# Kernel tuning notes

Hardware: AMD Instinct MI355X
Metric: run time of the kernel (lower is better)

Reference implementation:

```python
import jax, jax.numpy as jnp
import numpy as np

N = 16384
IN_FEATS = 256
OUT_FEATS = 256


def setup_inputs() -> dict:
    key = jax.random.key(0)
    k1, k2, k3, k4 = jax.random.split(key, 4)
    # dense (row-normalized-ish) adjacency; scaled so aggregated values stay O(1)
    graph = jax.random.uniform(k1, (N, N), dtype=jnp.float32) / N
    features = jax.random.normal(k2, (N, IN_FEATS), dtype=jnp.float32)
    # nn.Linear params: W [out, in], b [out]
    W = jax.random.normal(k3, (OUT_FEATS, IN_FEATS), dtype=jnp.float32) / np.sqrt(IN_FEATS)
    b = jax.random.normal(k4, (OUT_FEATS,), dtype=jnp.float32) * 0.01
    return {"graph": graph, "features": features, "W": W, "b": b}


def reference(graph, features, W, b):
    # h = graph @ features  (GCN-style dense neighbor aggregation)
    h = jnp.matmul(graph, features)            # [N, in_feats]
    # linear: h @ W.T + b
    h = jnp.einsum('ni,oi->no', h, W) + b      # [N, out_feats]
    # activation = relu (norm = None)
    return jax.nn.relu(h)
```

## Files before the change

### kernel.cpp

```cpp
#include <hip/hip_runtime.h>
#include <hip/hip_bf16.h>

typedef float f32x4 __attribute__((ext_vector_type(4)));
typedef short short8 __attribute__((ext_vector_type(8)));
typedef __bf16 bf16x8 __attribute__((ext_vector_type(8)));

#define N_TOT 16384
#define FEATS 256
#define BM 256
#define BK 32
#define KSPLIT 4
#define LDA (BK + 8)

static __device__ __forceinline__ ushort f2bf(float f) {
  union { __hip_bfloat16 b; ushort u; } cv;
  cv.b = __float2bfloat16(f);
  return cv.u;
}
static __device__ __forceinline__ float bf2f(ushort u) {
  union { unsigned int i; float f; } c;
  c.i = ((unsigned int)u) << 16;
  return c.f;
}

__global__ __launch_bounds__(256) void k_transpose(const float* __restrict__ feat,
                                                   ushort* __restrict__ fT) {
  __shared__ float tile[64][65];
  const int tx = threadIdx.x & 63, ty = threadIdx.x >> 6;
  const int k0 = blockIdx.x * 64, n0 = blockIdx.y * 64;
#pragma unroll
  for (int j = 0; j < 64; j += 4)
    tile[ty + j][tx] = feat[(size_t)(k0 + ty + j) * FEATS + n0 + tx];
  __syncthreads();
#pragma unroll
  for (int j = 0; j < 64; j += 4)
    fT[(size_t)(n0 + ty + j) * N_TOT + k0 + tx] = f2bf(tile[tx][ty + j]);
}

__global__ __launch_bounds__(256) void k_convw(const float* __restrict__ W,
                                               ushort* __restrict__ Wb) {
  int i = (blockIdx.x * 256 + threadIdx.x) * 4;
  float4 v = *(const float4*)(W + i);
  ushort4 h = { f2bf(v.x), f2bf(v.y), f2bf(v.z), f2bf(v.w) };
  *(ushort4*)(Wb + i) = h;
}

__global__ __launch_bounds__(512) void k_gemm1(const float* __restrict__ graph,
                                               const ushort* __restrict__ fT,
                                               ushort* __restrict__ parts) {
  __shared__ ushort Alds[2][BM][LDA];
  __shared__ ushort Blds[2][FEATS][LDA];
  const int tid = threadIdx.x;
  const int lane = tid & 63, w = tid >> 6;
  const int wm = w >> 2, wn = w & 3;
  const size_t m0 = (size_t)blockIdx.x * BM;
  const int kbase = blockIdx.y * (N_TOT / KSPLIT);
  const int nsteps = (N_TOT / KSPLIT) / BK;

  f32x4 acc[8][4] = {};

  auto stage = [&](int bf, int kk) {
#pragma unroll
    for (int i = 0; i < 4; ++i) {
      const int row = i * 64 + (tid >> 3);
      const int kq = (tid & 7) << 2;
      const float4 v = *(const float4*)(graph + (size_t)(m0 + row) * N_TOT + kk + kq);
      ushort4 h = { f2bf(v.x), f2bf(v.y), f2bf(v.z), f2bf(v.w) };
      *(ushort4*)&Alds[bf][row][kq] = h;
    }
    {
      const int n = tid >> 1;
      const int kq = (tid & 1) << 4;
      const short8 v0 = *(const short8*)(fT + (size_t)n * N_TOT + kk + kq);
      const short8 v1 = *(const short8*)(fT + (size_t)n * N_TOT + kk + kq + 8);
      *(short8*)&Blds[bf][n][kq] = v0;
      *(short8*)&Blds[bf][n][kq + 8] = v1;
    }
  };

  stage(0, kbase);
  __syncthreads();

  for (int step = 0; step < nsteps; ++step) {
    const int cur = step & 1;
    if (step + 1 < nsteps) stage(cur ^ 1, kbase + (step + 1) * BK);

    const int koff = (lane >> 4) << 3;
    const int rsel = lane & 15;
    short8 afr[8];
#pragma unroll
    for (int mf = 0; mf < 8; ++mf)
      afr[mf] = *(const short8*)&Alds[cur][wm * 128 + mf * 16 + rsel][koff];
    short8 bfr[4];
#pragma unroll
    for (int nf = 0; nf < 4; ++nf)
      bfr[nf] = *(const short8*)&Blds[cur][wn * 64 + nf * 16 + rsel][koff];
#pragma unroll
    for (int mf = 0; mf < 8; ++mf)
#pragma unroll
      for (int nf = 0; nf < 4; ++nf)
        acc[mf][nf] = __builtin_amdgcn_mfma_f32_16x16x32_bf16(
            __builtin_bit_cast(bf16x8, afr[mf]), __builtin_bit_cast(bf16x8, bfr[nf]),
            acc[mf][nf], 0, 0, 0);
    __syncthreads();
  }

  ushort* p = parts + (size_t)blockIdx.y * N_TOT * FEATS;
#pragma unroll
  for (int mf = 0; mf < 8; ++mf)
#pragma unroll
    for (int nf = 0; nf < 4; ++nf)
#pragma unroll
      for (int j = 0; j < 4; ++j) {
        const int row = wm * 128 + mf * 16 + ((lane >> 4) << 2) + j;
        const int col = wn * 64 + nf * 16 + (lane & 15);
        p[(m0 + row) * FEATS + col] = f2bf(acc[mf][nf][j]);
      }
}

__global__ __launch_bounds__(256) void k_gemm2(const ushort* __restrict__ parts,
                                               const ushort* __restrict__ Wb,
                                               const float* __restrict__ bias,
                                               float* __restrict__ out) {
  __shared__ ushort Al[64][264];
  __shared__ ushort Bl[FEATS][40];
  const int tid = threadIdx.x;
  const int lane = tid & 63, w = tid >> 6;
  const size_t m0 = (size_t)blockIdx.x * 64;

  for (int c = tid; c < 2048; c += 256) {
    const int row = c >> 5;
    const int k8 = (c & 31) << 3;
    const size_t off = (m0 + row) * FEATS + k8;
    float s[8] = {0, 0, 0, 0, 0, 0, 0, 0};
#pragma unroll
    for (int p = 0; p < KSPLIT; ++p) {
      const short8 v = *(const short8*)(parts + (size_t)p * N_TOT * FEATS + off);
#pragma unroll
      for (int j = 0; j < 8; ++j) s[j] += bf2f((ushort)v[j]);
    }
    short8 ov;
#pragma unroll
    for (int j = 0; j < 8; ++j) ov[j] = (short)f2bf(s[j]);
    *(short8*)&Al[row][k8] = ov;
  }

  f32x4 acc[16] = {};
  for (int kk = 0; kk < FEATS; kk += 32) {
    __syncthreads();
#pragma unroll
    for (int q = 0; q < 4; ++q) {
      const short8 v = *(const short8*)(Wb + (size_t)tid * FEATS + kk + q * 8);
      *(short8*)&Bl[tid][q * 8] = v;
    }
    __syncthreads();
    const int koff = (lane >> 4) << 3;
    const short8 af = *(const short8*)&Al[w * 16 + (lane & 15)][kk + koff];
#pragma unroll
    for (int nf = 0; nf < 16; ++nf) {
      const short8 bfv = *(const short8*)&Bl[nf * 16 + (lane & 15)][koff];
      acc[nf] = __builtin_amdgcn_mfma_f32_16x16x32_bf16(
          __builtin_bit_cast(bf16x8, af), __builtin_bit_cast(bf16x8, bfv),
          acc[nf], 0, 0, 0);
    }
  }

#pragma unroll
  for (int nf = 0; nf < 16; ++nf) {
    const int col = nf * 16 + (lane & 15);
    const float bc = bias[col];
#pragma unroll
    for (int j = 0; j < 4; ++j) {
      const int row = w * 16 + ((lane >> 4) << 2) + j;
      const float v = acc[nf][j] + bc;
      out[(m0 + row) * FEATS + col] = fmaxf(v, 0.0f);
    }
  }
}

extern "C" void kernel_launch(void* const* d_in, const int* in_sizes, int n_in,
                              void* d_out, int out_size, void* d_ws, size_t ws_size,
                              hipStream_t stream) {
  const float* graph = (const float*)d_in[0];
  const float* feat  = (const float*)d_in[1];
  const float* W     = (const float*)d_in[2];
  const float* bias  = (const float*)d_in[3];
  float* out = (float*)d_out;

  char* ws = (char*)d_ws;
  ushort* fT    = (ushort*)ws;
  ushort* Wb    = (ushort*)(ws + (size_t)8 * 1024 * 1024);
  ushort* parts = (ushort*)(ws + (size_t)8 * 1024 * 1024 + 131072);

  k_transpose<<<dim3(N_TOT / 64, FEATS / 64), 256, 0, stream>>>(feat, fT);
  k_convw<<<dim3(64), 256, 0, stream>>>(W, Wb);
  k_gemm1<<<dim3(N_TOT / BM, KSPLIT), 512, 0, stream>>>(graph, fT, parts);
  k_gemm2<<<dim3(N_TOT / 64), 256, 0, stream>>>(parts, Wb, bias, out);
}
```

Measured before the change: 300.3 us.

## Prefetch graph tiles two steps ahead through registers in aggregation GEMM

Rewrites the main loop of the first GEMM as a software pipeline. Global loads for tile t+2 are held in registers while tile t+1 is converted to bf16 and written into the alternate LDS buffer. Explicit s_barrier/waitcnt points, a sched_barrier and raised wave priority around the MFMA block are meant to overlap HBM reads of the fp32 adjacency with matrix math. It also requests two blocks per CU through launch bounds, which constrains registers and may cause spills given the 128-float accumulator. The grid is only 256 blocks, so the extra occupancy may not be used.

```diff
diff --git a/kernel.cpp b/kernel.cpp
--- a/kernel.cpp
+++ b/kernel.cpp
@@ -10,7 +10,8 @@
 #define BM 256
 #define BK 32
 #define KSPLIT 4
-#define LDA (BK + 8)
+#define LDA 40
+#define NSTEPS ((N_TOT / KSPLIT) / BK)
 
 static __device__ __forceinline__ ushort f2bf(float f) {
   union { __hip_bfloat16 b; ushort u; } cv;
@@ -45,9 +46,11 @@
   *(ushort4*)(Wb + i) = h;
 }
 
-__global__ __launch_bounds__(512) void k_gemm1(const float* __restrict__ graph,
-                                               const ushort* __restrict__ fT,
-                                               ushort* __restrict__ parts) {
+struct SRegs { float4 a[4]; uint4 b[2]; };
+
+__global__ __launch_bounds__(512, 2) void k_gemm1(const float* __restrict__ graph,
+                                                  const ushort* __restrict__ fT,
+                                                  ushort* __restrict__ parts) {
   __shared__ ushort Alds[2][BM][LDA];
   __shared__ ushort Blds[2][FEATS][LDA];
   const int tid = threadIdx.x;
@@ -55,54 +58,80 @@
   const int wm = w >> 2, wn = w & 3;
   const size_t m0 = (size_t)blockIdx.x * BM;
   const int kbase = blockIdx.y * (N_TOT / KSPLIT);
-  const int nsteps = (N_TOT / KSPLIT) / BK;
+
+  const float*  gA = graph + m0 * N_TOT + kbase;
+  const ushort* gB = fT + kbase;
 
   f32x4 acc[8][4] = {};
-
-  auto stage = [&](int bf, int kk) {
+  SRegs r0, r1;
+
+  auto issue = [&](SRegs& r, int t) {
+    const float*  a = gA + t * BK;
+    const ushort* b = gB + t * BK;
 #pragma unroll
     for (int i = 0; i < 4; ++i) {
-      const int row = i * 64 + (tid >> 3);
-      const int kq = (tid & 7) << 2;
-      const float4 v = *(const float4*)(graph + (size_t)(m0 + row) * N_TOT + kk + kq);
-      ushort4 h = { f2bf(v.x), f2bf(v.y), f2bf(v.z), f2bf(v.w) };
-      *(ushort4*)&Alds[bf][row][kq] = h;
-    }
-    {
-      const int n = tid >> 1;
-      const int kq = (tid & 1) << 4;
-      const short8 v0 = *(const short8*)(fT + (size_t)n * N_TOT + kk + kq);
-      const short8 v1 = *(const short8*)(fT + (size_t)n * N_TOT + kk + kq + 8);
-      *(short8*)&Blds[bf][n][kq] = v0;
-      *(short8*)&Blds[bf][n][kq + 8] = v1;
+      const int f4 = i * 512 + tid;
+      r.a[i] = *(const float4*)(a + (size_t)(f4 >> 3) * N_TOT + (f4 & 7) * 4);
+    }
+#pragma unroll
+    for (int i = 0; i < 2; ++i) {
+      const int f16 = i * 512 + tid;
+      r.b[i] = *(const uint4*)(b + (size_t)(f16 >> 2) * N_TOT + (f16 & 3) * 8);
     }
   };
-
-  stage(0, kbase);
-  __syncthreads();
-
-  for (int step = 0; step < nsteps; ++step) {
-    const int cur = step & 1;
-    if (step + 1 < nsteps) stage(cur ^ 1, kbase + (step + 1) * BK);
-
-    const int koff = (lane >> 4) << 3;
-    const int rsel = lane & 15;
-    short8 afr[8];
-#pragma unroll
-    for (int mf = 0; mf < 8; ++mf)
-      afr[mf] = *(const short8*)&Alds[cur][wm * 128 + mf * 16 + rsel][koff];
+  auto cwrite = [&](ushort (*Al)[LDA], ushort (*Bl)[LDA], SRegs& r) {
+#pragma unroll
+    for (int i = 0; i < 4; ++i) {
+      const int f4 = i * 512 + tid;
+      ushort4 h = { f2bf(r.a[i].x), f2bf(r.a[i].y), f2bf(r.a[i].z), f2bf(r.a[i].w) };
+      *(ushort4*)&Al[f4 >> 3][(f4 & 7) * 4] = h;
+    }
+#pragma unroll
+    for (int i = 0; i < 2; ++i) {
+      const int f16 = i * 512 + tid;
+      *(uint4*)&Bl[f16 >> 2][(f16 & 3) * 8] = r.b[i];
+    }
+  };
+
+  issue(r0, 0);
+  issue(r1, 1);
+  cwrite(Alds[0], Blds[0], r0);
+  asm volatile("s_waitcnt lgkmcnt(0)" ::: "memory");
+  __builtin_amdgcn_s_barrier();
+
+  const int koff = (lane >> 4) << 3;
+  const int rsel = lane & 15;
+
+  auto tile = [&](ushort (*Ac)[LDA], ushort (*Bc)[LDA],
+                  ushort (*An)[LDA], ushort (*Bn)[LDA],
+                  SRegs& rw, SRegs& ri, int t) {
+    if (t + 1 < NSTEPS) cwrite(An, Bn, rw);
+    if (t + 2 < NSTEPS) issue(ri, t + 2);
+    __builtin_amdgcn_sched_barrier(0);
     short8 bfr[4];
 #pragma unroll
     for (int nf = 0; nf < 4; ++nf)
-      bfr[nf] = *(const short8*)&Blds[cur][wn * 64 + nf * 16 + rsel][koff];
-#pragma unroll
-    for (int mf = 0; mf < 8; ++mf)
+      bfr[nf] = *(const short8*)&Bc[wn * 64 + nf * 16 + rsel][koff];
+    asm volatile("s_waitcnt lgkmcnt(0)" ::: "memory");
+    __builtin_amdgcn_s_barrier();
+    __builtin_amdgcn_s_setprio(1);
+#pragma unroll
+    for (int mf = 0; mf < 8; ++mf) {
+      const short8 afr = *(const short8*)&Ac[wm * 128 + mf * 16 + rsel][koff];
 #pragma unroll
       for (int nf = 0; nf < 4; ++nf)
         acc[mf][nf] = __builtin_amdgcn_mfma_f32_16x16x32_bf16(
-            __builtin_bit_cast(bf16x8, afr[mf]), __builtin_bit_cast(bf16x8, bfr[nf]),
+            __builtin_bit_cast(bf16x8, afr), __builtin_bit_cast(bf16x8, bfr[nf]),
             acc[mf][nf], 0, 0, 0);
-    __syncthreads();
+    }
+    __builtin_amdgcn_s_setprio(0);
+    asm volatile("s_waitcnt lgkmcnt(0)" ::: "memory");
+    __builtin_amdgcn_s_barrier();
+  };
+
+  for (int t = 0; t < NSTEPS; t += 2) {
+    tile(Alds[0], Blds[0], Alds[1], Blds[1], r1, r0, t);
+    tile(Alds[1], Blds[1], Alds[0], Blds[0], r0, r1, t + 1);
   }
 
   ushort* p = parts + (size_t)blockIdx.y * N_TOT * FEATS;
```

Result: faster. 289.0 us (-3.8%).

## Stage gemm1 tiles via direct global-to-LDS loads with XOR swizzle, convert A in registers

Applied to the files above, without the earlier changes.

Replaces the register-staged loads of graph and fT with global_load_lds 16-byte async copies straight into LDS. The fp32 graph tile is kept in fp32 in LDS and converted to bf16 at fragment-read time. The layout uses an XOR swizzle instead of padding to avoid bank conflicts, and launch bounds request two blocks per CU. The goal is to remove VGPR staging and load latency from the main loop so loads overlap MFMA. The cost is twice the LDS footprint for A and conversion work repeated per warp.

```diff
diff --git a/kernel.cpp b/kernel.cpp
--- a/kernel.cpp
+++ b/kernel.cpp
@@ -10,7 +10,9 @@
 #define BM 256
 #define BK 32
 #define KSPLIT 4
-#define LDA (BK + 8)
+#define NSTEPS ((N_TOT / KSPLIT) / BK)
+#define LDSA_BYTES (BM * 128)
+#define LDSB_BYTES (FEATS * 64)
 
 static __device__ __forceinline__ ushort f2bf(float f) {
   union { __hip_bfloat16 b; ushort u; } cv;
@@ -21,6 +23,11 @@
   union { unsigned int i; float f; } c;
   c.i = ((unsigned int)u) << 16;
   return c.f;
+}
+static __device__ __forceinline__ void gload_lds16(const void* g, void* l) {
+  __builtin_amdgcn_global_load_lds((const __attribute__((address_space(1))) unsigned int*)g,
+                                   (__attribute__((address_space(3))) unsigned int*)l,
+                                   16, 0, 0);
 }
 
 __global__ __launch_bounds__(256) void k_transpose(const float* __restrict__ feat,
@@ -45,63 +52,71 @@
   *(ushort4*)(Wb + i) = h;
 }
 
-__global__ __launch_bounds__(512) void k_gemm1(const float* __restrict__ graph,
-                                               const ushort* __restrict__ fT,
-                                               ushort* __restrict__ parts) {
-  __shared__ ushort Alds[2][BM][LDA];
-  __shared__ ushort Blds[2][FEATS][LDA];
+__global__ __launch_bounds__(512, 2) void k_gemm1(const float* __restrict__ graph,
+                                                  const ushort* __restrict__ fT,
+                                                  ushort* __restrict__ parts) {
+  __shared__ char lds[2][LDSA_BYTES + LDSB_BYTES];
   const int tid = threadIdx.x;
   const int lane = tid & 63, w = tid >> 6;
   const int wm = w >> 2, wn = w & 3;
   const size_t m0 = (size_t)blockIdx.x * BM;
   const int kbase = blockIdx.y * (N_TOT / KSPLIT);
-  const int nsteps = (N_TOT / KSPLIT) / BK;
+
+  auto stage = [&](int bf, int t) {
+    const int k0 = kbase + t * BK;
+    char* ldsA = &lds[bf][0];
+    char* ldsB = &lds[bf][LDSA_BYTES];
+#pragma unroll
+    for (int j = 0; j < 4; ++j) {
+      const int r0 = w * 32 + j * 8;
+      const int row = r0 + (lane >> 3);
+      const int c = (lane & 7) ^ (row & 7);
+      gload_lds16(graph + (m0 + row) * (size_t)N_TOT + k0 + c * 4, ldsA + r0 * 128);
+    }
+#pragma unroll
+    for (int j = 0; j < 2; ++j) {
+      const int r0 = w * 32 + j * 16;
+      const int row = r0 + (lane >> 2);
+      const int c = (lane & 3) ^ (row & 3);
+      gload_lds16(fT + (size_t)row * N_TOT + k0 + c * 8, ldsB + r0 * 64);
+    }
+  };
 
   f32x4 acc[8][4] = {};
-
-  auto stage = [&](int bf, int kk) {
-#pragma unroll
-    for (int i = 0; i < 4; ++i) {
-      const int row = i * 64 + (tid >> 3);
-      const int kq = (tid & 7) << 2;
-      const float4 v = *(const float4*)(graph + (size_t)(m0 + row) * N_TOT + kk + kq);
-      ushort4 h = { f2bf(v.x), f2bf(v.y), f2bf(v.z), f2bf(v.w) };
-      *(ushort4*)&Alds[bf][row][kq] = h;
-    }
-    {
-      const int n = tid >> 1;
-      const int kq = (tid & 1) << 4;
-      const short8 v0 = *(const short8*)(fT + (size_t)n * N_TOT + kk + kq);
-      const short8 v1 = *(const short8*)(fT + (size_t)n * N_TOT + kk + kq + 8);
-      *(short8*)&Blds[bf][n][kq] = v0;
-      *(short8*)&Blds[bf][n][kq + 8] = v1;
-    }
-  };
-
-  stage(0, kbase);
+  const int rsel = lane & 15;
+  const int kg = lane >> 4;
+
+  stage(0, 0);
   __syncthreads();
 
-  for (int step = 0; step < nsteps; ++step) {
-    const int cur = step & 1;
-    if (step + 1 < nsteps) stage(cur ^ 1, kbase + (step + 1) * BK);
-
-    const int koff = (lane >> 4) << 3;
-    const int rsel = lane & 15;
-    short8 afr[8];
-#pragma unroll
-    for (int mf = 0; mf < 8; ++mf)
-      afr[mf] = *(const short8*)&Alds[cur][wm * 128 + mf * 16 + rsel][koff];
+  for (int t = 0; t < NSTEPS; ++t) {
+    const int cur = t & 1;
+    if (t + 1 < NSTEPS) stage(cur ^ 1, t + 1);
+    __builtin_amdgcn_sched_barrier(0);
+
+    const char* Ab = &lds[cur][0];
+    const char* Bb = &lds[cur][LDSA_BYTES];
     short8 bfr[4];
 #pragma unroll
-    for (int nf = 0; nf < 4; ++nf)
-      bfr[nf] = *(const short8*)&Blds[cur][wn * 64 + nf * 16 + rsel][koff];
-#pragma unroll
-    for (int mf = 0; mf < 8; ++mf)
+    for (int nf = 0; nf < 4; ++nf) {
+      const int row = wn * 64 + nf * 16 + rsel;
+      const int c = kg ^ (row & 3);
+      bfr[nf] = *(const short8*)(Bb + row * 64 + c * 16);
+    }
+#pragma unroll
+    for (int mf = 0; mf < 8; ++mf) {
+      const int row = wm * 128 + mf * 16 + rsel;
+      const int cb = (row & 7);
+      const float4 a0 = *(const float4*)(Ab + row * 128 + ((kg * 2) ^ cb) * 16);
+      const float4 a1 = *(const float4*)(Ab + row * 128 + ((kg * 2 + 1) ^ cb) * 16);
+      short8 af = { (short)f2bf(a0.x), (short)f2bf(a0.y), (short)f2bf(a0.z), (short)f2bf(a0.w),
+                    (short)f2bf(a1.x), (short)f2bf(a1.y), (short)f2bf(a1.z), (short)f2bf(a1.w) };
 #pragma unroll
       for (int nf = 0; nf < 4; ++nf)
         acc[mf][nf] = __builtin_amdgcn_mfma_f32_16x16x32_bf16(
-            __builtin_bit_cast(bf16x8, afr[mf]), __builtin_bit_cast(bf16x8, bfr[nf]),
+            __builtin_bit_cast(bf16x8, af), __builtin_bit_cast(bf16x8, bfr[nf]),
             acc[mf][nf], 0, 0, 0);
+    }
     __syncthreads();
   }
 
```

After: 310.4 us. 1.03x slower.
